# Optimization experiments

Measured on AMD Instinct MI355X. Metric: run time of the kernel, lower is better.

The kernel has to match this reference:

```python
import jax, jax.numpy as jnp
import numpy as np

B, N, D_MODEL, H, BLK = 2, 2048, 1024, 16, 128
TB = N // BLK  # 16 blocks per side
NEG = -1e30


def setup_inputs() -> dict:
    key = jax.random.key(0)
    kq, kk, kv, kb = jax.random.split(key, 4)
    q = jax.random.normal(kq, (B, N, D_MODEL), jnp.float32)
    k = jax.random.normal(kk, (B, N, D_MODEL), jnp.float32)
    v = jax.random.normal(kv, (B, N, D_MODEL), jnp.float32)
    tau = jnp.float32(1.0)
    mask = jnp.ones((B, 1, N, N), jnp.int32)
    block_sparse_mask = jax.random.randint(kb, (TB, TB), 0, 2).astype(jnp.int32)
    return {"q": q, "k": k, "v": v, "tau": tau, "mask": mask,
            "block_sparse_mask": block_sparse_mask}


def reference(q, k, v, tau, mask, block_sparse_mask):
    # Equivalent closed form of the tiled online-softmax loop (dropout p=0, eval
    # mode): processed blocks accumulate exactly masked softmax(tau*QK^T/sqrt(dk))@V;
    # rows whose every block is skipped keep O=0, l=0, m=-inf.
    Bq, Nq, D = q.shape
    d_k = D // H
    qh = q.reshape(Bq, Nq, H, d_k).transpose(0, 2, 1, 3)  # (B,H,N,dk)
    kh = k.reshape(Bq, Nq, H, d_k).transpose(0, 2, 1, 3)
    vh = v.reshape(Bq, Nq, H, d_k).transpose(0, 2, 1, 3)

    S = tau * jnp.einsum('bhqd,bhkd->bhqk', qh, kh) / np.sqrt(d_k).astype(np.float32)

    # expand block-sparse pattern to token resolution (N,N)
    bs = jnp.repeat(jnp.repeat(block_sparse_mask, BLK, axis=0), BLK, axis=1)
    allowed = (mask != 0) & (bs != 0)  # (B,1,N,N), broadcasts over heads

    S_m = jnp.where(allowed, S, NEG)
    m = jnp.max(S_m, axis=-1, keepdims=True)            # (B,H,N,1)
    P = jnp.exp(S_m - m) * allowed.astype(S.dtype)      # masked exp-weights
    l = jnp.sum(P, axis=-1, keepdims=True)              # (B,H,N,1)
    Ov = jnp.einsum('bhqk,bhkd->bhqd', P, vh)
    O = Ov / jnp.where(l > 0, l, 1.0)

    has_any = jnp.any(allowed, axis=-1, keepdims=True)  # (B,1,N,1)
    m_out = jnp.where(has_any, m, -jnp.inf)
    O_out = O.transpose(0, 2, 1, 3).reshape(Bq, Nq, D)
    return O_out, l, m_out
```

## Files before the change

kernel.cpp:

```cpp
#include <hip/hip_runtime.h>
#include <hip/hip_bf16.h>

#define B_   2
#define N_   2048
#define DM_  1024
#define H_   16
#define DK_  64
#define BLK_ 128
#define TB_  16

typedef unsigned short u16;
typedef unsigned int   u32;
using bf16x8 = __attribute__((ext_vector_type(8))) __bf16;
using f32x4  = __attribute__((ext_vector_type(4))) float;

#define KPAD 72
#define VPAD 136
#define PPAD 136
#define OPAD 68

__device__ __forceinline__ u32 pack_bf16(float a, float b) {
  __hip_bfloat162 h = __float22bfloat162_rn(make_float2(a, b));
  u32 u; __builtin_memcpy(&u, &h, 4); return u;
}
__device__ __forceinline__ bf16x8 pack8(float4 f0, float4 f1, float sc) {
  u32 w[4];
  w[0] = pack_bf16(f0.x * sc, f0.y * sc); w[1] = pack_bf16(f0.z * sc, f0.w * sc);
  w[2] = pack_bf16(f1.x * sc, f1.y * sc); w[3] = pack_bf16(f1.z * sc, f1.w * sc);
  bf16x8 r; __builtin_memcpy(&r, w, 16); return r;
}

__global__ void kv_convert(const float* __restrict__ k, const float* __restrict__ v,
                           u16* __restrict__ kb, u16* __restrict__ vt) {
  __shared__ u16 tile[BLK_][DK_ + 2];
  const int b = blockIdx.z, h = blockIdx.y, nb = blockIdx.x;
  const int t = threadIdx.x;
  const int rr = t >> 4, cc = (t & 15) * 4;
  {
    const float* kg = k + ((size_t)(b * N_ + nb * BLK_)) * DM_ + h * DK_;
    u16* kd = kb + ((size_t)((b * H_ + h) * N_) + nb * BLK_) * DK_;
#pragma unroll
    for (int i = 0; i < 8; ++i) {
      const int r = rr + i * 16;
      const float4 f = *(const float4*)(kg + (size_t)r * DM_ + cc);
      *(uint2*)(kd + r * DK_ + cc) = make_uint2(pack_bf16(f.x, f.y), pack_bf16(f.z, f.w));
    }
  }
  {
    const float* vg = v + ((size_t)(b * N_ + nb * BLK_)) * DM_ + h * DK_;
#pragma unroll
    for (int i = 0; i < 8; ++i) {
      const int r = rr + i * 16;
      const float4 f = *(const float4*)(vg + (size_t)r * DM_ + cc);
      *(u32*)(&tile[r][cc])     = pack_bf16(f.x, f.y);
      *(u32*)(&tile[r][cc + 2]) = pack_bf16(f.z, f.w);
    }
    __syncthreads();
    const int d = t & 63, n0 = (t >> 6) * 32;
    u16* og = vt + ((size_t)(b * H_ + h) * DK_ + d) * N_ + nb * BLK_ + n0;
#pragma unroll
    for (int j = 0; j < 32; j += 8) {
      u16 tmp[8];
#pragma unroll
      for (int x = 0; x < 8; ++x) tmp[x] = tile[n0 + j + x][d];
      uint4 w; __builtin_memcpy(&w, tmp, 16);
      *(uint4*)(og + j) = w;
    }
  }
}

__global__ void mask_flags_kernel(const int* __restrict__ mask, const int* __restrict__ bs,
                                  int* __restrict__ flags) {
  const int blk = blockIdx.x;
  const int kb = blk % TB_, qb = (blk / TB_) % TB_, b = blk / (TB_ * TB_);
  const int t = threadIdx.x;
  const int* mg = mask + (size_t)b * N_ * N_ + (size_t)(qb * BLK_) * N_ + kb * BLK_;
  int all1 = 1, any1 = 0;
  for (int i = t; i < BLK_ * BLK_ / 4; i += 256) {
    const int r = i >> 5, c = (i & 31) * 4;
    const int4 mv = *(const int4*)(mg + (size_t)r * N_ + c);
    all1 &= (mv.x != 0) & (mv.y != 0) & (mv.z != 0) & (mv.w != 0);
    any1 |= (mv.x != 0) | (mv.y != 0) | (mv.z != 0) | (mv.w != 0);
  }
  __shared__ int sAll[4], sAny[4];
  const int wv = t >> 6;
  const int wAll = __all(all1), wAny = __any(any1);
  if ((t & 63) == 0) { sAll[wv] = wAll; sAny[wv] = wAny; }
  __syncthreads();
  if (t == 0) {
    const int A = sAll[0] & sAll[1] & sAll[2] & sAll[3];
    const int O = sAny[0] | sAny[1] | sAny[2] | sAny[3];
    int f = 0;
    if (bs[qb * TB_ + kb] != 0 && O) f = A ? 1 : 2;
    flags[blk] = f;
  }
}

#define ISSUE_KV(blk_) do {                                                     \
    const u16* ks_ = kbase + (size_t)(blk_) * BLK_ * DK_;                       \
    const u16* vs_ = vbase + (blk_) * BLK_;                                     \
    _Pragma("unroll")                                                           \
    for (int j_ = 0; j_ < 4; ++j_) {                                            \
      const int i_ = t + 256 * j_;                                              \
      kr[j_] = *(const uint4*)(ks_ + i_ * 8);                                   \
      vr[j_] = *(const uint4*)(vs_ + (size_t)(i_ >> 4) * N_ + (i_ & 15) * 8);   \
    }                                                                           \
  } while (0)

__global__ __launch_bounds__(256, 2)
void attn_kernel(const float* __restrict__ q_, const u16* __restrict__ kb_,
                 const u16* __restrict__ vt, const float* __restrict__ tau_p,
                 const int* __restrict__ mask, const int* __restrict__ flags,
                 float* __restrict__ o_out, float* __restrict__ l_out,
                 float* __restrict__ m_out) {
  __shared__ __align__(16) u16 lds[BLK_ * KPAD + DK_ * VPAD + BLK_ * PPAD];
  u16* Ks  = lds;
  u16* Vts = Ks + BLK_ * KPAD;
  u16* Ps  = Vts + DK_ * VPAD;
  float* Os = (float*)lds;

  const int idx = blockIdx.x;
  const int bh = idx & 31, qb128 = idx >> 5;
  const int b = bh >> 4, h = bh & 15;
  const int t = threadIdx.x;
  const int wave = t >> 6, lane = t & 63, quad = lane >> 4, col = lane & 15;

  const int* flg = flags + (b * TB_ + qb128) * TB_;
  u32 actmask = 0, mixmask = 0;
#pragma unroll
  for (int i = 0; i < TB_; ++i) {
    const int f = flg[i];
    actmask |= (f != 0) ? (1u << i) : 0u;
    mixmask |= (f == 2) ? (1u << i) : 0u;
  }

  const u16* kbase = kb_ + (size_t)(b * H_ + h) * N_ * DK_;
  const u16* vbase = vt + (size_t)(b * H_ + h) * DK_ * N_;

  uint4 kr[4], vr[4];
  u32 rem = actmask;
  int cur = -1;
  if (rem) { cur = (int)__builtin_ctz(rem); rem &= rem - 1; ISSUE_KV(cur); }

  int qg[2];
  qg[0] = qb128 * BLK_ + wave * 32 + col;
  qg[1] = qg[0] + 16;

  const float qscale = tau_p[0] * 0.125f * 1.44269504f;
  bf16x8 bq[2][2];
#pragma unroll
  for (int nt = 0; nt < 2; ++nt) {
    const float* qr = q_ + ((size_t)(b * N_ + qg[nt])) * DM_ + h * DK_;
#pragma unroll
    for (int half = 0; half < 2; ++half) {
      const float4 f0 = *(const float4*)(qr + half * 32 + quad * 8);
      const float4 f1 = *(const float4*)(qr + half * 32 + quad * 8 + 4);
      bq[nt][half] = pack8(f0, f1, qscale);
    }
  }

  float m_run[2]  = {-INFINITY, -INFINITY};
  float m_true[2] = {-INFINITY, -INFINITY};
  float l_run[2] = {0.f, 0.f};
  f32x4 oacc[2][4];
#pragma unroll
  for (int nt = 0; nt < 2; ++nt)
#pragma unroll
    for (int mt = 0; mt < 4; ++mt) oacc[nt][mt] = (f32x4){0.f, 0.f, 0.f, 0.f};

  while (cur >= 0) {
    const int mix = (mixmask >> cur) & 1;

    __syncthreads();
#pragma unroll
    for (int j = 0; j < 4; ++j) {
      const int i = t + 256 * j;
      *(uint4*)(Ks + (i >> 3) * KPAD + (i & 7) * 8) = kr[j];
      *(uint4*)(Vts + (i >> 4) * VPAD + (i & 15) * 8) = vr[j];
    }
    __syncthreads();

    int nxt = -1;
    if (rem) { nxt = (int)__builtin_ctz(rem); rem &= rem - 1; ISSUE_KV(nxt); }

#pragma unroll
    for (int nt = 0; nt < 2; ++nt) {
      f32x4 st[8];
      __builtin_amdgcn_s_setprio(1);
#pragma unroll
      for (int kt = 0; kt < 8; ++kt) {
        const bf16x8 a0 = *(const bf16x8*)(Ks + (kt * 16 + col) * KPAD + quad * 8);
        const bf16x8 a1 = *(const bf16x8*)(Ks + (kt * 16 + col) * KPAD + 32 + quad * 8);
        f32x4 c = (f32x4){0.f, 0.f, 0.f, 0.f};
        c = __builtin_amdgcn_mfma_f32_16x16x32_bf16(a0, bq[nt][0], c, 0, 0, 0);
        c = __builtin_amdgcn_mfma_f32_16x16x32_bf16(a1, bq[nt][1], c, 0, 0, 0);
        st[kt] = c;
      }
      __builtin_amdgcn_s_setprio(0);
      if (mix) {
        const int* mg = mask + (size_t)b * N_ * N_ + (size_t)qg[nt] * N_ + cur * BLK_;
#pragma unroll
        for (int kt = 0; kt < 8; ++kt) {
          const int4 mv = *(const int4*)(mg + kt * 16 + quad * 4);
          if (!mv.x) st[kt][0] = -1e30f;
          if (!mv.y) st[kt][1] = -1e30f;
          if (!mv.z) st[kt][2] = -1e30f;
          if (!mv.w) st[kt][3] = -1e30f;
        }
      }
      float mx = -INFINITY;
#pragma unroll
      for (int kt = 0; kt < 8; ++kt)
        mx = fmaxf(mx, fmaxf(fmaxf(st[kt][0], st[kt][1]), fmaxf(st[kt][2], st[kt][3])));
      mx = fmaxf(mx, __shfl_xor(mx, 16, 64));
      mx = fmaxf(mx, __shfl_xor(mx, 32, 64));
      m_true[nt] = fmaxf(m_true[nt], mx);

      const float mold = m_run[nt];
      float mnew = mold;
      if (!__all(mx <= mold + 8.f)) {
        mnew = fmaxf(mold, mx);
        const float alpha = __builtin_amdgcn_exp2f(mold - mnew);
        l_run[nt] *= alpha;
#pragma unroll
        for (int mt = 0; mt < 4; ++mt)
#pragma unroll
          for (int r = 0; r < 4; ++r) oacc[nt][mt][r] *= alpha;
        m_run[nt] = mnew;
      }

      const int qloc = wave * 32 + nt * 16 + col;
      float s = 0.f;
      if (!mix) {
#pragma unroll
        for (int kt = 0; kt < 8; ++kt) {
          const float p0 = __builtin_amdgcn_exp2f(st[kt][0] - mnew);
          const float p1 = __builtin_amdgcn_exp2f(st[kt][1] - mnew);
          const float p2 = __builtin_amdgcn_exp2f(st[kt][2] - mnew);
          const float p3 = __builtin_amdgcn_exp2f(st[kt][3] - mnew);
          s += (p0 + p1) + (p2 + p3);
          *(uint2*)(Ps + qloc * PPAD + kt * 16 + quad * 4) =
              make_uint2(pack_bf16(p0, p1), pack_bf16(p2, p3));
        }
      } else {
#pragma unroll
        for (int kt = 0; kt < 8; ++kt) {
          const float p0 = st[kt][0] <= -1e29f ? 0.f : __builtin_amdgcn_exp2f(st[kt][0] - mnew);
          const float p1 = st[kt][1] <= -1e29f ? 0.f : __builtin_amdgcn_exp2f(st[kt][1] - mnew);
          const float p2 = st[kt][2] <= -1e29f ? 0.f : __builtin_amdgcn_exp2f(st[kt][2] - mnew);
          const float p3 = st[kt][3] <= -1e29f ? 0.f : __builtin_amdgcn_exp2f(st[kt][3] - mnew);
          s += (p0 + p1) + (p2 + p3);
          *(uint2*)(Ps + qloc * PPAD + kt * 16 + quad * 4) =
              make_uint2(pack_bf16(p0, p1), pack_bf16(p2, p3));
        }
      }
      s += __shfl_xor(s, 16, 64);
      s += __shfl_xor(s, 32, 64);
      l_run[nt] += s;
    }

    __builtin_amdgcn_s_setprio(1);
#pragma unroll
    for (int ks = 0; ks < 4; ++ks) {
      bf16x8 bfrag[2];
#pragma unroll
      for (int nt = 0; nt < 2; ++nt)
        bfrag[nt] = *(const bf16x8*)(Ps + (wave * 32 + nt * 16 + col) * PPAD + ks * 32 + quad * 8);
#pragma unroll
      for (int mt = 0; mt < 4; ++mt) {
        const bf16x8 av = *(const bf16x8*)(Vts + (mt * 16 + col) * VPAD + ks * 32 + quad * 8);
#pragma unroll
        for (int nt = 0; nt < 2; ++nt)
          oacc[nt][mt] = __builtin_amdgcn_mfma_f32_16x16x32_bf16(av, bfrag[nt], oacc[nt][mt], 0, 0, 0);
      }
    }
    __builtin_amdgcn_s_setprio(0);
    cur = nxt;
  }

  __syncthreads();
#pragma unroll
  for (int nt = 0; nt < 2; ++nt) {
    const float inv = l_run[nt] > 0.f ? 1.f / l_run[nt] : 1.f;
    const int qloc = wave * 32 + nt * 16 + col;
#pragma unroll
    for (int mt = 0; mt < 4; ++mt) {
      float4 w = make_float4(oacc[nt][mt][0] * inv, oacc[nt][mt][1] * inv,
                             oacc[nt][mt][2] * inv, oacc[nt][mt][3] * inv);
      *(float4*)(Os + qloc * OPAD + mt * 16 + quad * 4) = w;
    }
  }
  __syncthreads();
  float* ob = o_out + ((size_t)(b * N_ + qb128 * BLK_)) * DM_ + h * DK_;
#pragma unroll
  for (int j = 0; j < 8; ++j) {
    const int i = t + 256 * j;
    const int r = i >> 4, c4 = (i & 15) * 4;
    const float4 w = *(const float4*)(Os + r * OPAD + c4);
    *(float4*)(ob + (size_t)r * DM_ + c4) = w;
  }
  if (quad == 0) {
#pragma unroll
    for (int nt = 0; nt < 2; ++nt) {
      const size_t oi = (size_t)(b * H_ + h) * N_ + qg[nt];
      const float lv = l_run[nt] > 0.f
          ? l_run[nt] * __builtin_amdgcn_exp2f(m_run[nt] - m_true[nt]) : 0.f;
      l_out[oi] = lv;
      m_out[oi] = l_run[nt] > 0.f ? m_true[nt] * 0.69314718056f : -INFINITY;
    }
  }
}

extern "C" void kernel_launch(void* const* d_in, const int* in_sizes, int n_in,
                              void* d_out, int out_size, void* d_ws, size_t ws_size,
                              hipStream_t stream) {
  const float* q   = (const float*)d_in[0];
  const float* k   = (const float*)d_in[1];
  const float* v   = (const float*)d_in[2];
  const float* tau = (const float*)d_in[3];
  const int* mask  = (const int*)d_in[4];
  const int* bs    = (const int*)d_in[5];
  float* out = (float*)d_out;

  const size_t plane = (size_t)B_ * H_ * N_ * DK_;
  u16* kb = (u16*)d_ws;
  u16* vt = kb + plane;
  int* flags = (int*)(vt + plane);

  kv_convert<<<dim3(N_ / BLK_, H_, B_), 256, 0, stream>>>(k, v, kb, vt);
  mask_flags_kernel<<<B_ * TB_ * TB_, 256, 0, stream>>>(mask, bs, flags);

  float* o_out = out;
  float* l_out = out + (size_t)B_ * N_ * DM_;
  float* m_out = l_out + (size_t)B_ * H_ * N_;
  attn_kernel<<<dim3(TB_ * 32), 256, 0, stream>>>(q, kb, vt, tau, mask, flags,
                                                  o_out, l_out, m_out);
}
```

Before: 193.4 us.

## Double-buffer K/V in LDS via async global_load_lds with swizzled block images

After: 171.6 us. -11.3%, faster.

```diff
diff --git a/kernel.cpp b/kernel.cpp
--- a/kernel.cpp
+++ b/kernel.cpp
@@ -14,9 +14,6 @@
 using bf16x8 = __attribute__((ext_vector_type(8))) __bf16;
 using f32x4  = __attribute__((ext_vector_type(4))) float;
 
-#define KPAD 72
-#define VPAD 136
-#define PPAD 136
 #define OPAD 68
 
 __device__ __forceinline__ u32 pack_bf16(float a, float b) {
@@ -31,19 +28,21 @@
 }
 
 __global__ void kv_convert(const float* __restrict__ k, const float* __restrict__ v,
-                           u16* __restrict__ kb, u16* __restrict__ vt) {
+                           u16* __restrict__ kimg, u16* __restrict__ vimg) {
   __shared__ u16 tile[BLK_][DK_ + 2];
   const int b = blockIdx.z, h = blockIdx.y, nb = blockIdx.x;
   const int t = threadIdx.x;
+  const size_t obase = ((size_t)((b * H_ + h) * TB_ + nb)) * 8192;
   const int rr = t >> 4, cc = (t & 15) * 4;
   {
     const float* kg = k + ((size_t)(b * N_ + nb * BLK_)) * DM_ + h * DK_;
-    u16* kd = kb + ((size_t)((b * H_ + h) * N_) + nb * BLK_) * DK_;
+    u16* kd = kimg + obase;
 #pragma unroll
     for (int i = 0; i < 8; ++i) {
       const int r = rr + i * 16;
       const float4 f = *(const float4*)(kg + (size_t)r * DM_ + cc);
-      *(uint2*)(kd + r * DK_ + cc) = make_uint2(pack_bf16(f.x, f.y), pack_bf16(f.z, f.w));
+      const int so = ((((cc >> 3) ^ (r & 7)) << 3) | (cc & 4));
+      *(uint2*)(kd + r * 64 + so) = make_uint2(pack_bf16(f.x, f.y), pack_bf16(f.z, f.w));
     }
   }
   {
@@ -57,14 +56,15 @@
     }
     __syncthreads();
     const int d = t & 63, n0 = (t >> 6) * 32;
-    u16* og = vt + ((size_t)(b * H_ + h) * DK_ + d) * N_ + nb * BLK_ + n0;
+    u16* og = vimg + obase + d * 128;
 #pragma unroll
     for (int j = 0; j < 32; j += 8) {
       u16 tmp[8];
 #pragma unroll
       for (int x = 0; x < 8; ++x) tmp[x] = tile[n0 + j + x][d];
       uint4 w; __builtin_memcpy(&w, tmp, 16);
-      *(uint4*)(og + j) = w;
+      const int chunk = (n0 + j) >> 3;
+      *(uint4*)(og + ((chunk ^ (d & 7)) << 3)) = w;
     }
   }
 }
@@ -96,27 +96,29 @@
   }
 }
 
-#define ISSUE_KV(blk_) do {                                                     \
-    const u16* ks_ = kbase + (size_t)(blk_) * BLK_ * DK_;                       \
-    const u16* vs_ = vbase + (blk_) * BLK_;                                     \
-    _Pragma("unroll")                                                           \
-    for (int j_ = 0; j_ < 4; ++j_) {                                            \
-      const int i_ = t + 256 * j_;                                              \
-      kr[j_] = *(const uint4*)(ks_ + i_ * 8);                                   \
-      vr[j_] = *(const uint4*)(vs_ + (size_t)(i_ >> 4) * N_ + (i_ & 15) * 8);   \
-    }                                                                           \
+#define STAGE(blk_, bi_) do {                                                        \
+    const u16* ksrc_ = kpl + (size_t)(blk_) * 8192 + wave * 2048 + lane * 8;         \
+    const u16* vsrc_ = vpl + (size_t)(blk_) * 8192 + wave * 2048 + lane * 8;         \
+    u16* kdst_ = lds + (bi_) * 8192 + wave * 2048;                                   \
+    u16* vdst_ = lds + 16384 + (bi_) * 8192 + wave * 2048;                           \
+    _Pragma("unroll")                                                                \
+    for (int i2_ = 0; i2_ < 4; ++i2_) {                                              \
+      __builtin_amdgcn_global_load_lds(                                              \
+          (const __attribute__((address_space(1))) void*)(ksrc_ + i2_ * 512),        \
+          (__attribute__((address_space(3))) void*)(kdst_ + i2_ * 512), 16, 0, 0);   \
+      __builtin_amdgcn_global_load_lds(                                              \
+          (const __attribute__((address_space(1))) void*)(vsrc_ + i2_ * 512),        \
+          (__attribute__((address_space(3))) void*)(vdst_ + i2_ * 512), 16, 0, 0);   \
+    }                                                                                \
   } while (0)
 
 __global__ __launch_bounds__(256, 2)
-void attn_kernel(const float* __restrict__ q_, const u16* __restrict__ kb_,
-                 const u16* __restrict__ vt, const float* __restrict__ tau_p,
+void attn_kernel(const float* __restrict__ q_, const u16* __restrict__ kimg,
+                 const u16* __restrict__ vimg, const float* __restrict__ tau_p,
                  const int* __restrict__ mask, const int* __restrict__ flags,
                  float* __restrict__ o_out, float* __restrict__ l_out,
                  float* __restrict__ m_out) {
-  __shared__ __align__(16) u16 lds[BLK_ * KPAD + DK_ * VPAD + BLK_ * PPAD];
-  u16* Ks  = lds;
-  u16* Vts = Ks + BLK_ * KPAD;
-  u16* Ps  = Vts + DK_ * VPAD;
+  __shared__ __align__(16) u16 lds[4 * 8192];
   float* Os = (float*)lds;
 
   const int idx = blockIdx.x;
@@ -134,13 +136,12 @@
     mixmask |= (f == 2) ? (1u << i) : 0u;
   }
 
-  const u16* kbase = kb_ + (size_t)(b * H_ + h) * N_ * DK_;
-  const u16* vbase = vt + (size_t)(b * H_ + h) * DK_ * N_;
-
-  uint4 kr[4], vr[4];
+  const u16* kpl = kimg + (size_t)(b * H_ + h) * TB_ * 8192;
+  const u16* vpl = vimg + (size_t)(b * H_ + h) * TB_ * 8192;
+
   u32 rem = actmask;
   int cur = -1;
-  if (rem) { cur = (int)__builtin_ctz(rem); rem &= rem - 1; ISSUE_KV(cur); }
+  if (rem) { cur = (int)__builtin_ctz(rem); rem &= rem - 1; STAGE(cur, 0); }
 
   int qg[2];
   qg[0] = qb128 * BLK_ + wave * 32 + col;
@@ -168,20 +169,22 @@
 #pragma unroll
     for (int mt = 0; mt < 4; ++mt) oacc[nt][mt] = (f32x4){0.f, 0.f, 0.f, 0.f};
 
+  const int s8 = col & 7;
+  const int a0o = (quad ^ s8) << 3;
+  const int q2 = quad >> 1;
+
+  int bufi = 0;
   while (cur >= 0) {
+    __syncthreads();
+
+    int nxt = -1;
+    if (rem) { nxt = (int)__builtin_ctz(rem); rem &= rem - 1; STAGE(nxt, bufi ^ 1); }
+
     const int mix = (mixmask >> cur) & 1;
-
-    __syncthreads();
-#pragma unroll
-    for (int j = 0; j < 4; ++j) {
-      const int i = t + 256 * j;
-      *(uint4*)(Ks + (i >> 3) * KPAD + (i & 7) * 8) = kr[j];
-      *(uint4*)(Vts + (i >> 4) * VPAD + (i & 15) * 8) = vr[j];
-    }
-    __syncthreads();
-
-    int nxt = -1;
-    if (rem) { nxt = (int)__builtin_ctz(rem); rem &= rem - 1; ISSUE_KV(nxt); }
+    const u16* KsB = lds + bufi * 8192;
+    const u16* VtB = lds + 16384 + bufi * 8192;
+
+    u32 pw[2][16];
 
 #pragma unroll
     for (int nt = 0; nt < 2; ++nt) {
@@ -189,8 +192,9 @@
       __builtin_amdgcn_s_setprio(1);
 #pragma unroll
       for (int kt = 0; kt < 8; ++kt) {
-        const bf16x8 a0 = *(const bf16x8*)(Ks + (kt * 16 + col) * KPAD + quad * 8);
-        const bf16x8 a1 = *(const bf16x8*)(Ks + (kt * 16 + col) * KPAD + 32 + quad * 8);
+        const u16* krow = KsB + (kt * 16 + col) * 64;
+        const bf16x8 a0 = *(const bf16x8*)(krow + a0o);
+        const bf16x8 a1 = *(const bf16x8*)(krow + (a0o ^ 32));
         f32x4 c = (f32x4){0.f, 0.f, 0.f, 0.f};
         c = __builtin_amdgcn_mfma_f32_16x16x32_bf16(a0, bq[nt][0], c, 0, 0, 0);
         c = __builtin_amdgcn_mfma_f32_16x16x32_bf16(a1, bq[nt][1], c, 0, 0, 0);
@@ -229,7 +233,6 @@
         m_run[nt] = mnew;
       }
 
-      const int qloc = wave * 32 + nt * 16 + col;
       float s = 0.f;
       if (!mix) {
 #pragma unroll
@@ -239,8 +242,8 @@
           const float p2 = __builtin_amdgcn_exp2f(st[kt][2] - mnew);
           const float p3 = __builtin_amdgcn_exp2f(st[kt][3] - mnew);
           s += (p0 + p1) + (p2 + p3);
-          *(uint2*)(Ps + qloc * PPAD + kt * 16 + quad * 4) =
-              make_uint2(pack_bf16(p0, p1), pack_bf16(p2, p3));
+          pw[nt][kt * 2 + 0] = pack_bf16(p0, p1);
+          pw[nt][kt * 2 + 1] = pack_bf16(p2, p3);
         }
       } else {
 #pragma unroll
@@ -250,8 +253,8 @@
           const float p2 = st[kt][2] <= -1e29f ? 0.f : __builtin_amdgcn_exp2f(st[kt][2] - mnew);
           const float p3 = st[kt][3] <= -1e29f ? 0.f : __builtin_amdgcn_exp2f(st[kt][3] - mnew);
           s += (p0 + p1) + (p2 + p3);
-          *(uint2*)(Ps + qloc * PPAD + kt * 16 + quad * 4) =
-              make_uint2(pack_bf16(p0, p1), pack_bf16(p2, p3));
+          pw[nt][kt * 2 + 0] = pack_bf16(p0, p1);
+          pw[nt][kt * 2 + 1] = pack_bf16(p2, p3);
         }
       }
       s += __shfl_xor(s, 16, 64);
@@ -259,22 +262,42 @@
       l_run[nt] += s;
     }
 
-    __builtin_amdgcn_s_setprio(1);
 #pragma unroll
     for (int ks = 0; ks < 4; ++ks) {
       bf16x8 bfrag[2];
 #pragma unroll
-      for (int nt = 0; nt < 2; ++nt)
-        bfrag[nt] = *(const bf16x8*)(Ps + (wave * 32 + nt * 16 + col) * PPAD + ks * 32 + quad * 8);
+      for (int nt = 0; nt < 2; ++nt) {
+        const u32 wA0 = pw[nt][4 * ks + 0], wA1 = pw[nt][4 * ks + 1];
+        const u32 wB0 = pw[nt][4 * ks + 2], wB1 = pw[nt][4 * ks + 3];
+        const u32 a0 = q2 ? wB0 : wA0;
+        const u32 a1 = q2 ? wB1 : wA1;
+        const u32 b0 = q2 ? wA0 : wB0;
+        const u32 b1 = q2 ? wA1 : wB1;
+        const u32 x16_0 = __shfl_xor(a0, 16, 64);
+        const u32 x16_1 = __shfl_xor(a1, 16, 64);
+        const u32 x32_0 = __shfl_xor(b0, 32, 64);
+        const u32 x32_1 = __shfl_xor(b1, 32, 64);
+        const u32 x48_0 = __shfl_xor(b0, 48, 64);
+        const u32 x48_1 = __shfl_xor(b1, 48, 64);
+        u32 wv[4];
+        wv[0] = (quad & 2) ? ((quad & 1) ? x16_0 : x32_0) : ((quad & 1) ? x48_0 : a0);
+        wv[1] = (quad & 2) ? ((quad & 1) ? x16_1 : x32_1) : ((quad & 1) ? x48_1 : a1);
+        wv[2] = (quad & 2) ? ((quad & 1) ? a0 : x48_0) : ((quad & 1) ? x32_0 : x16_0);
+        wv[3] = (quad & 2) ? ((quad & 1) ? a1 : x48_1) : ((quad & 1) ? x32_1 : x16_1);
+        __builtin_memcpy(&bfrag[nt], wv, 16);
+      }
+      __builtin_amdgcn_s_setprio(1);
 #pragma unroll
       for (int mt = 0; mt < 4; ++mt) {
-        const bf16x8 av = *(const bf16x8*)(Vts + (mt * 16 + col) * VPAD + ks * 32 + quad * 8);
-#pragma unroll
-        for (int nt = 0; nt < 2; ++nt)
-          oacc[nt][mt] = __builtin_amdgcn_mfma_f32_16x16x32_bf16(av, bfrag[nt], oacc[nt][mt], 0, 0, 0);
-      }
-    }
-    __builtin_amdgcn_s_setprio(0);
+        const bf16x8 av =
+            *(const bf16x8*)(VtB + (mt * 16 + col) * 128 + (((ks * 4 + quad) ^ s8) << 3));
+        oacc[0][mt] = __builtin_amdgcn_mfma_f32_16x16x32_bf16(av, bfrag[0], oacc[0][mt], 0, 0, 0);
+        oacc[1][mt] = __builtin_amdgcn_mfma_f32_16x16x32_bf16(av, bfrag[1], oacc[1][mt], 0, 0, 0);
+      }
+      __builtin_amdgcn_s_setprio(0);
+    }
+
+    bufi ^= 1;
     cur = nxt;
   }
 
@@ -323,16 +346,16 @@
   float* out = (float*)d_out;
 
   const size_t plane = (size_t)B_ * H_ * N_ * DK_;
-  u16* kb = (u16*)d_ws;
-  u16* vt = kb + plane;
-  int* flags = (int*)(vt + plane);
-
-  kv_convert<<<dim3(N_ / BLK_, H_, B_), 256, 0, stream>>>(k, v, kb, vt);
+  u16* kimg = (u16*)d_ws;
+  u16* vimg = kimg + plane;
+  int* flags = (int*)(vimg + plane);
+
+  kv_convert<<<dim3(TB_, H_, B_), 256, 0, stream>>>(k, v, kimg, vimg);
   mask_flags_kernel<<<B_ * TB_ * TB_, 256, 0, stream>>>(mask, bs, flags);
 
   float* o_out = out;
   float* l_out = out + (size_t)B_ * N_ * DM_;
   float* m_out = l_out + (size_t)B_ * H_ * N_;
-  attn_kernel<<<dim3(TB_ * 32), 256, 0, stream>>>(q, kb, vt, tau, mask, flags,
+  attn_kernel<<<dim3(TB_ * 32), 256, 0, stream>>>(q, kimg, vimg, tau, mask, flags,
                                                   o_out, l_out, m_out);
 }
```
